# Performance work log

Measured on AMD Instinct MI355X. Metric: run time of the kernel, lower is better.

The kernel has to match this reference:

```python
import jax, jax.numpy as jnp
import numpy as np
import math

B, S, D_MODEL = 4, 2048, 1024
H, D_HEAD = 16, 64
INIT_RANGE = 0.02


def setup_inputs() -> dict:
    key = jax.random.key(0)
    ks = jax.random.split(key, 10)
    x = jax.random.normal(ks[0], (B, S, D_MODEL), dtype=jnp.float32)
    # torch Linear(in,out): y = x @ W.T + b. We store weights pre-transposed as [H, in, out].
    u = lambda k, shape: jax.random.uniform(k, shape, dtype=jnp.float32, minval=-INIT_RANGE, maxval=INIT_RANGE)
    wq = u(ks[1], (H, D_MODEL, D_HEAD))
    wk = u(ks[2], (H, D_MODEL, D_HEAD))
    wv = u(ks[3], (H, D_MODEL, D_HEAD))
    wo = u(ks[4], (H, D_HEAD, D_MODEL))
    # biases: torch default init is uniform(-1/sqrt(fan_in), 1/sqrt(fan_in)); values don't matter for correctness harness
    bq = u(ks[5], (H, D_HEAD))
    bk = u(ks[6], (H, D_HEAD))
    bv = u(ks[7], (H, D_HEAD))
    bo = u(ks[8], (H, D_MODEL))
    return {"normalized_resid_pre": x, "wq": wq, "bq": bq, "wk": wk, "bk": bk,
            "wv": wv, "bv": bv, "wo": wo, "bo": bo}


def reference(normalized_resid_pre, wq, bq, wk, bk, wv, bv, wo, bo):
    x = normalized_resid_pre  # [B, S, D]
    # Batched multi-head QKV projections (original does a python loop per head)
    q = jnp.einsum('bsd,hde->bhse', x, wq) + bq[None, :, None, :]  # [B,H,S,dh]
    k = jnp.einsum('bsd,hde->bhse', x, wk) + bk[None, :, None, :]
    v = jnp.einsum('bsd,hde->bhse', x, wv) + bv[None, :, None, :]
    scale = 1.0 / math.sqrt(D_HEAD)  # cfg.global_d_head, used unconditionally
    scores = jnp.einsum('bhse,bhte->bhst', q, k) * scale  # [B,H,S,S], non-causal
    attn = jax.nn.softmax(scores, axis=-1)
    heads = jnp.einsum('bhst,bhte->bhse', attn, v)  # [B,H,S,dh]
    # per-head output projections, summed over heads (= sum of per-head Linear outputs)
    out = jnp.einsum('bhse,hed->bsd', heads, wo) + jnp.sum(bo, axis=0)[None, None, :]
    return out
```

## Files before the change

### kernel.cpp

```cpp
#include <hip/hip_runtime.h>
#include <hip/hip_bf16.h>
#include <math.h>


typedef __attribute__((ext_vector_type(8))) short bf16x8;
typedef __attribute__((ext_vector_type(4))) float f32x4;

#define GLDS16(gsrc, lbase) \
    __builtin_amdgcn_global_load_lds((const __attribute__((address_space(1))) void*)(gsrc), \
                                     (__attribute__((address_space(3))) void*)(lbase), 16, 0, 0)

static __device__ __forceinline__ ushort f2bf(float f) {
    __bf16 h = (__bf16)f;
    return *reinterpret_cast<ushort*>(&h);
}
static __device__ __forceinline__ unsigned pk_bf16(float a, float b) {
    return (unsigned)f2bf(a) | ((unsigned)f2bf(b) << 16);
}
static __device__ __forceinline__ float clampf(float v) {
    return fminf(fmaxf(v, -1e30f), 1e30f);
}

__global__ void cvt_x(const float* __restrict__ x, ushort* __restrict__ xb) {
    int idx = blockIdx.x * 256 + threadIdx.x;
    float4 a = ((const float4*)x)[idx * 2];
    float4 b = ((const float4*)x)[idx * 2 + 1];
    uint4 o;
    o.x = pk_bf16(a.x, a.y);
    o.y = pk_bf16(a.z, a.w);
    o.z = pk_bf16(b.x, b.y);
    o.w = pk_bf16(b.z, b.w);
    ((uint4*)xb)[idx] = o;
}

__global__ void pack_wqkv(const float* __restrict__ wq, const float* __restrict__ wk,
                          const float* __restrict__ wv, const float* __restrict__ bq,
                          const float* __restrict__ bk, const float* __restrict__ bv,
                          ushort* __restrict__ WT, float* __restrict__ biasc) {
    __shared__ __align__(16) ushort Lt[64][72];
    int bid = blockIdx.x;
    int kt = bid & 15, h = (bid >> 4) & 15, proj = bid >> 8;
    const float* w  = (proj == 0) ? wq : (proj == 1) ? wk : wv;
    const float* bb = (proj == 0) ? bq : (proj == 1) ? bk : bv;
    const float scale = (proj == 0) ? 0.18033688011112042f : 1.0f;
    int t = threadIdx.x;
    int e = t & 63, kr = t >> 6;
    const float* src = w + (size_t)h * 65536 + (size_t)kt * 64 * 64 + e;
    #pragma unroll
    for (int i = 0; i < 16; ++i) {
        int kl = kr * 16 + i;
        Lt[e][kl] = f2bf(src[(size_t)kl * 64] * scale);
    }
    if (kt == 0 && t < 64) biasc[proj * 1024 + h * 64 + t] = bb[h * 64 + t] * scale;
    __syncthreads();
    int eo = t >> 2, kc = (t & 3) * 16;
    size_t dst = (size_t)(proj * 1024 + h * 64 + eo) * 1024 + kt * 64 + kc;
    *(bf16x8*)(WT + dst)     = *(const bf16x8*)(&Lt[eo][kc]);
    *(bf16x8*)(WT + dst + 8) = *(const bf16x8*)(&Lt[eo][kc + 8]);
}
__global__ void pack_wo(const float* __restrict__ wo, const float* __restrict__ bo,
                        ushort* __restrict__ WoT, float* __restrict__ biaso) {
    __shared__ __align__(16) ushort Lt[64][72];
    int bid = blockIdx.x;
    int het = bid & 15, dt = bid >> 4;
    int t = threadIdx.x;
    int dl = t & 63, hw = t >> 6;
    #pragma unroll
    for (int i = 0; i < 16; ++i) {
        int hel = hw * 16 + i;
        Lt[dl][hel] = f2bf(wo[(size_t)(het * 64 + hel) * 1024 + dt * 64 + dl]);
    }
    if (het == 0 && t < 64) {
        int d = dt * 64 + t;
        float s = 0.f;
        for (int hh = 0; hh < 16; ++hh) s += bo[hh * 1024 + d];
        biaso[d] = s;
    }
    __syncthreads();
    int do_ = t >> 2, hc = (t & 3) * 16;
    size_t dst = (size_t)(dt * 64 + do_) * 1024 + het * 64 + hc;
    *(bf16x8*)(WoT + dst)     = *(const bf16x8*)(&Lt[do_][hc]);
    *(bf16x8*)(WoT + dst + 8) = *(const bf16x8*)(&Lt[do_][hc + 8]);
}

__global__ void transpose_v(const ushort* __restrict__ C1x, ushort* __restrict__ Vt) {
    __shared__ ushort Lt[64][72];
    int st = blockIdx.x, b = blockIdx.y, h = blockIdx.z;
    int t = threadIdx.x;
    int r = t >> 3, c = (t & 7) * 8;
    #pragma unroll
    for (int i = 0; i < 2; ++i) {
        int sl = r + i * 32;
        bf16x8 v = *(const bf16x8*)(C1x + (size_t)(b * 2048 + st * 64 + sl) * 3072
                                    + 2048 + h * 64 + c);
        int pos = ((sl & 15) << 2) | (sl >> 4);
        #pragma unroll
        for (int j = 0; j < 8; ++j) Lt[c + j][pos] = (ushort)v[j];
    }
    __syncthreads();
    int e = t >> 2, ch = (t & 3) * 16;
    size_t dst = (size_t)b * (1024 * 2048) + (size_t)(h * 64 + e) * 2048 + st * 64 + ch;
    *(bf16x8*)(Vt + dst)     = *(const bf16x8*)(&Lt[e][ch]);
    *(bf16x8*)(Vt + dst + 8) = *(const bf16x8*)(&Lt[e][ch + 8]);
}

__global__ __launch_bounds__(256, 2) void gemm_bt(
    const ushort* __restrict__ A, const ushort* __restrict__ Bt,
    const float* __restrict__ bias, ushort* __restrict__ C,
    float* __restrict__ Cf, int M, int N, int K, int ldc)
{
    __shared__ __align__(16) ushort Al[128][64];
    __shared__ __align__(16) ushort Bl[128][64];
    const int t = threadIdx.x;
    const int lane = t & 63, wave = t >> 6;
    const int wr = wave >> 1, wc = wave & 1;
    const int quad = lane >> 4, l16 = lane & 15;
    const int row0 = blockIdx.x * 128, col0 = blockIdx.y * 128;
    const int sr = t >> 3;
    const int scx = ((t & 7) ^ (sr & 7)) * 8;
    const int xk = l16 & 7;

    f32x4 acc[4][4] = {};

    for (int kt = 0; kt < K; kt += 64) {
        char* abase = (char*)Al + wave * 1024;
        char* bbase = (char*)Bl + wave * 1024;
        const ushort* ag = A  + (size_t)(row0 + sr) * K + kt + scx;
        const ushort* bg = Bt + (size_t)(col0 + sr) * K + kt + scx;
        #pragma unroll
        for (int i = 0; i < 4; ++i) {
            GLDS16(ag + (size_t)i * 32 * K, abase + i * 4096);
            GLDS16(bg + (size_t)i * 32 * K, bbase + i * 4096);
        }
        __syncthreads();
        #pragma unroll
        for (int ks = 0; ks < 2; ++ks) {
            bf16x8 a[4], b[4];
            #pragma unroll
            for (int mi = 0; mi < 4; ++mi)
                a[mi] = *(const bf16x8*)(&Al[wr * 64 + mi * 16 + l16][((ks * 4 + quad) ^ xk) * 8]);
            #pragma unroll
            for (int ni = 0; ni < 4; ++ni)
                b[ni] = *(const bf16x8*)(&Bl[wc * 64 + ni * 16 + l16][((ks * 4 + quad) ^ xk) * 8]);
            #pragma unroll
            for (int mi = 0; mi < 4; ++mi)
                #pragma unroll
                for (int ni = 0; ni < 4; ++ni)
                    acc[mi][ni] = __builtin_amdgcn_mfma_f32_16x16x32_bf16(a[mi], b[ni], acc[mi][ni], 0, 0, 0);
        }
        __syncthreads();
    }
    #pragma unroll
    for (int mi = 0; mi < 4; ++mi) {
        int rowb = row0 + wr * 64 + mi * 16 + quad * 4;
        #pragma unroll
        for (int ni = 0; ni < 4; ++ni) {
            int col = col0 + wc * 64 + ni * 16 + l16;
            float bs = bias ? bias[col] : 0.f;
            #pragma unroll
            for (int r = 0; r < 4; ++r) {
                float v = clampf(acc[mi][ni][r] + bs);
                int row = rowb + r;
                if (Cf) Cf[(size_t)row * ldc + col] = v;
                else    C [(size_t)row * ldc + col] = f2bf(v);
            }
        }
    }
}

__global__ __launch_bounds__(256, 2) void attn(
    const ushort* __restrict__ QK, const ushort* __restrict__ Vt, ushort* __restrict__ O)
{
    __shared__ __align__(16) ushort Kl[64][64];
    __shared__ __align__(16) ushort Vl[64][64];
    __shared__ __align__(16) ushort Pl[4][32][72];
    const int qt = blockIdx.x, b = blockIdx.y, h = blockIdx.z;
    const int t = threadIdx.x, lane = t & 63, wave = t >> 6;
    const int quad = lane >> 4, l16 = lane & 15;
    const int rowq0 = b * 2048 + qt * 128 + wave * 32;
    const int sr = t >> 3;
    const int scx = ((t & 7) ^ (sr & 7)) * 8;
    const int xk = l16 & 7;

    bf16x8 qf[2][2];
    #pragma unroll
    for (int mi = 0; mi < 2; ++mi)
        #pragma unroll
        for (int ks = 0; ks < 2; ++ks)
            qf[mi][ks] = *(const bf16x8*)(QK + (size_t)(rowq0 + mi * 16 + l16) * 3072
                                          + h * 64 + ks * 32 + quad * 8);

    f32x4 of[2][4] = {};
    float lpart[2][4] = {};

    const ushort* kg0 = QK + (size_t)(b * 2048 + sr) * 3072 + 1024 + h * 64 + scx;
    const ushort* vg0 = Vt + (size_t)b * (1024 * 2048) + (size_t)(h * 64 + sr) * 2048 + scx;

    for (int kt = 0; kt < 2048; kt += 64) {
        {
            char* kbase = (char*)Kl + wave * 1024;
            char* vbase = (char*)Vl + wave * 1024;
            const ushort* kg = kg0 + (size_t)kt * 3072;
            const ushort* vg = vg0 + kt;
            GLDS16(kg, kbase);
            GLDS16(kg + (size_t)32 * 3072, kbase + 4096);
            GLDS16(vg, vbase);
            GLDS16(vg + 32 * 2048, vbase + 4096);
        }
        __syncthreads();

        f32x4 sf[2][4] = {};
        #pragma unroll
        for (int ks = 0; ks < 2; ++ks) {
            bf16x8 kb[4];
            #pragma unroll
            for (int nt = 0; nt < 4; ++nt)
                kb[nt] = *(const bf16x8*)(&Kl[nt * 16 + l16][((ks * 4 + quad) ^ xk) * 8]);
            #pragma unroll
            for (int mi = 0; mi < 2; ++mi)
                #pragma unroll
                for (int nt = 0; nt < 4; ++nt)
                    sf[mi][nt] = __builtin_amdgcn_mfma_f32_16x16x32_bf16(qf[mi][ks], kb[nt], sf[mi][nt], 0, 0, 0);
        }

        #pragma unroll
        for (int mi = 0; mi < 2; ++mi) {
            #pragma unroll
            for (int r = 0; r < 4; ++r) {
                float p0 = exp2f(sf[mi][0][r]);
                float p1 = exp2f(sf[mi][1][r]);
                float p2 = exp2f(sf[mi][2][r]);
                float p3 = exp2f(sf[mi][3][r]);
                lpart[mi][r] += (p0 + p1) + (p2 + p3);
                int prw = mi * 16 + quad * 4 + r;
                uint2 pk;
                pk.x = pk_bf16(p0, p1);
                pk.y = pk_bf16(p2, p3);
                *(uint2*)(&Pl[wave][prw][l16 * 4]) = pk;
            }
        }

        #pragma unroll
        for (int ks = 0; ks < 2; ++ks) {
            bf16x8 pa[2];
            #pragma unroll
            for (int mi = 0; mi < 2; ++mi)
                pa[mi] = *(const bf16x8*)(&Pl[wave][mi * 16 + l16][ks * 32 + quad * 8]);
            #pragma unroll
            for (int nt = 0; nt < 4; ++nt) {
                bf16x8 vb = *(const bf16x8*)(&Vl[nt * 16 + l16][((ks * 4 + quad) ^ xk) * 8]);
                #pragma unroll
                for (int mi = 0; mi < 2; ++mi)
                    of[mi][nt] = __builtin_amdgcn_mfma_f32_16x16x32_bf16(pa[mi], vb, of[mi][nt], 0, 0, 0);
            }
        }
        __syncthreads();
    }

    #pragma unroll
    for (int mi = 0; mi < 2; ++mi) {
        #pragma unroll
        for (int r = 0; r < 4; ++r) {
            float l = lpart[mi][r];
            #pragma unroll
            for (int d = 1; d < 16; d <<= 1) l += __shfl_xor(l, d, 64);
            float inv = 1.0f / fmaxf(l, 1e-30f);
            int row = rowq0 + mi * 16 + quad * 4 + r;
            #pragma unroll
            for (int nt = 0; nt < 4; ++nt)
                O[(size_t)row * 1024 + h * 64 + nt * 16 + l16] = f2bf(clampf(of[mi][nt][r] * inv));
        }
    }
}

extern "C" void kernel_launch(void* const* d_in, const int* in_sizes, int n_in,
                              void* d_out, int out_size, void* d_ws, size_t ws_size,
                              hipStream_t stream) {
    const float* x  = (const float*)d_in[0];
    const float* wq = (const float*)d_in[1];
    const float* bq = (const float*)d_in[2];
    const float* wk = (const float*)d_in[3];
    const float* bk = (const float*)d_in[4];
    const float* wv = (const float*)d_in[5];
    const float* bv = (const float*)d_in[6];
    const float* wo = (const float*)d_in[7];
    const float* bo = (const float*)d_in[8];

    char* ws = (char*)d_ws;
    const size_t MB = 1024 * 1024;
    ushort* xb    = (ushort*)(ws);
    ushort* WqkvT = (ushort*)(ws + 16 * MB);
    ushort* WoT   = (ushort*)(ws + 22 * MB);
    float*  biasc = (float*) (ws + 24 * MB);
    float*  biaso = (float*) (ws + 24 * MB + 64 * 1024);
    ushort* C1x   = (ushort*)(ws + 25 * MB);
    ushort* Vt    = (ushort*)(ws + 73 * MB);
    ushort* Obuf  = xb;

    cvt_x    <<<4096, 256, 0, stream>>>(x, xb);
    pack_wqkv<<<768, 256, 0, stream>>>(wq, wk, wv, bq, bk, bv, WqkvT, biasc);
    pack_wo  <<<256, 256, 0, stream>>>(wo, bo, WoT, biaso);

    gemm_bt<<<dim3(64, 24), 256, 0, stream>>>(xb, WqkvT, biasc, C1x, nullptr,
                                              8192, 3072, 1024, 3072);
    transpose_v<<<dim3(32, 4, 16), 256, 0, stream>>>(C1x, Vt);
    attn<<<dim3(16, 4, 16), 256, 0, stream>>>(C1x, Vt, Obuf);
    gemm_bt<<<dim3(64, 8), 256, 0, stream>>>(Obuf, WoT, biaso, nullptr, (float*)d_out,
                                             8192, 1024, 1024, 1024);
}
```

Measured before the change: 323.6 us.

## Enlarge attention blocks to 8 waves with 128-key tiles; fuse prep kernels

The attention kernel now runs 512 threads (8 waves) per block, covering 256 query rows, and stages 128 keys of K and V per iteration, processed in two 64-key halves. Each loaded K/V tile is shared by twice as many query rows, and there are half as many block-wide barriers per key. The three preprocessing kernels (x conversion, QKV weight pack, Wo pack) are merged into one launch to cut launch overhead. The trade-offs are more LDS per block, a new swizzle for the wider V tile, and fewer blocks in the grid, which may reduce occupancy.

Result: slower. 457.2 us (+41.3%).

```diff
diff --git a/kernel.cpp b/kernel.cpp
--- a/kernel.cpp
+++ b/kernel.cpp
@@ -21,66 +21,70 @@
     return fminf(fmaxf(v, -1e30f), 1e30f);
 }
 
-__global__ void cvt_x(const float* __restrict__ x, ushort* __restrict__ xb) {
-    int idx = blockIdx.x * 256 + threadIdx.x;
-    float4 a = ((const float4*)x)[idx * 2];
-    float4 b = ((const float4*)x)[idx * 2 + 1];
-    uint4 o;
-    o.x = pk_bf16(a.x, a.y);
-    o.y = pk_bf16(a.z, a.w);
-    o.z = pk_bf16(b.x, b.y);
-    o.w = pk_bf16(b.z, b.w);
-    ((uint4*)xb)[idx] = o;
-}
-
-__global__ void pack_wqkv(const float* __restrict__ wq, const float* __restrict__ wk,
-                          const float* __restrict__ wv, const float* __restrict__ bq,
-                          const float* __restrict__ bk, const float* __restrict__ bv,
-                          ushort* __restrict__ WT, float* __restrict__ biasc) {
+__global__ void prep(const float* __restrict__ x, ushort* __restrict__ xb,
+                     const float* __restrict__ wq, const float* __restrict__ wk,
+                     const float* __restrict__ wv, const float* __restrict__ bq,
+                     const float* __restrict__ bk, const float* __restrict__ bv,
+                     ushort* __restrict__ WT, float* __restrict__ biasc,
+                     const float* __restrict__ wo, const float* __restrict__ bo,
+                     ushort* __restrict__ WoT, float* __restrict__ biaso) {
     __shared__ __align__(16) ushort Lt[64][72];
     int bid = blockIdx.x;
-    int kt = bid & 15, h = (bid >> 4) & 15, proj = bid >> 8;
-    const float* w  = (proj == 0) ? wq : (proj == 1) ? wk : wv;
-    const float* bb = (proj == 0) ? bq : (proj == 1) ? bk : bv;
-    const float scale = (proj == 0) ? 0.18033688011112042f : 1.0f;
     int t = threadIdx.x;
-    int e = t & 63, kr = t >> 6;
-    const float* src = w + (size_t)h * 65536 + (size_t)kt * 64 * 64 + e;
-    #pragma unroll
-    for (int i = 0; i < 16; ++i) {
-        int kl = kr * 16 + i;
-        Lt[e][kl] = f2bf(src[(size_t)kl * 64] * scale);
-    }
-    if (kt == 0 && t < 64) biasc[proj * 1024 + h * 64 + t] = bb[h * 64 + t] * scale;
-    __syncthreads();
-    int eo = t >> 2, kc = (t & 3) * 16;
-    size_t dst = (size_t)(proj * 1024 + h * 64 + eo) * 1024 + kt * 64 + kc;
-    *(bf16x8*)(WT + dst)     = *(const bf16x8*)(&Lt[eo][kc]);
-    *(bf16x8*)(WT + dst + 8) = *(const bf16x8*)(&Lt[eo][kc + 8]);
-}
-__global__ void pack_wo(const float* __restrict__ wo, const float* __restrict__ bo,
-                        ushort* __restrict__ WoT, float* __restrict__ biaso) {
-    __shared__ __align__(16) ushort Lt[64][72];
-    int bid = blockIdx.x;
-    int het = bid & 15, dt = bid >> 4;
-    int t = threadIdx.x;
-    int dl = t & 63, hw = t >> 6;
-    #pragma unroll
-    for (int i = 0; i < 16; ++i) {
-        int hel = hw * 16 + i;
-        Lt[dl][hel] = f2bf(wo[(size_t)(het * 64 + hel) * 1024 + dt * 64 + dl]);
-    }
-    if (het == 0 && t < 64) {
-        int d = dt * 64 + t;
-        float s = 0.f;
-        for (int hh = 0; hh < 16; ++hh) s += bo[hh * 1024 + d];
-        biaso[d] = s;
-    }
-    __syncthreads();
-    int do_ = t >> 2, hc = (t & 3) * 16;
-    size_t dst = (size_t)(dt * 64 + do_) * 1024 + het * 64 + hc;
-    *(bf16x8*)(WoT + dst)     = *(const bf16x8*)(&Lt[do_][hc]);
-    *(bf16x8*)(WoT + dst + 8) = *(const bf16x8*)(&Lt[do_][hc + 8]);
+    if (bid < 4096) {
+        int idx = bid * 256 + t;
+        float4 a = ((const float4*)x)[idx * 2];
+        float4 b = ((const float4*)x)[idx * 2 + 1];
+        uint4 o;
+        o.x = pk_bf16(a.x, a.y);
+        o.y = pk_bf16(a.z, a.w);
+        o.z = pk_bf16(b.x, b.y);
+        o.w = pk_bf16(b.z, b.w);
+        ((uint4*)xb)[idx] = o;
+        return;
+    }
+    bid -= 4096;
+    if (bid < 768) {
+        int kt = bid & 15, h = (bid >> 4) & 15, proj = bid >> 8;
+        const float* w  = (proj == 0) ? wq : (proj == 1) ? wk : wv;
+        const float* bb = (proj == 0) ? bq : (proj == 1) ? bk : bv;
+        const float scale = (proj == 0) ? 0.18033688011112042f : 1.0f;
+        int e = t & 63, kr = t >> 6;
+        const float* src = w + (size_t)h * 65536 + (size_t)kt * 64 * 64 + e;
+        #pragma unroll
+        for (int i = 0; i < 16; ++i) {
+            int kl = kr * 16 + i;
+            Lt[e][kl] = f2bf(src[(size_t)kl * 64] * scale);
+        }
+        if (kt == 0 && t < 64) biasc[proj * 1024 + h * 64 + t] = bb[h * 64 + t] * scale;
+        __syncthreads();
+        int eo = t >> 2, kc = (t & 3) * 16;
+        size_t dst = (size_t)(proj * 1024 + h * 64 + eo) * 1024 + kt * 64 + kc;
+        *(bf16x8*)(WT + dst)     = *(const bf16x8*)(&Lt[eo][kc]);
+        *(bf16x8*)(WT + dst + 8) = *(const bf16x8*)(&Lt[eo][kc + 8]);
+        return;
+    }
+    bid -= 768;
+    {
+        int het = bid & 15, dt = bid >> 4;
+        int dl = t & 63, hw = t >> 6;
+        #pragma unroll
+        for (int i = 0; i < 16; ++i) {
+            int hel = hw * 16 + i;
+            Lt[dl][hel] = f2bf(wo[(size_t)(het * 64 + hel) * 1024 + dt * 64 + dl]);
+        }
+        if (het == 0 && t < 64) {
+            int d = dt * 64 + t;
+            float s = 0.f;
+            for (int hh = 0; hh < 16; ++hh) s += bo[hh * 1024 + d];
+            biaso[d] = s;
+        }
+        __syncthreads();
+        int do_ = t >> 2, hc = (t & 3) * 16;
+        size_t dst = (size_t)(dt * 64 + do_) * 1024 + het * 64 + hc;
+        *(bf16x8*)(WoT + dst)     = *(const bf16x8*)(&Lt[do_][hc]);
+        *(bf16x8*)(WoT + dst + 8) = *(const bf16x8*)(&Lt[do_][hc + 8]);
+    }
 }
 
 __global__ void transpose_v(const ushort* __restrict__ C1x, ushort* __restrict__ Vt) {
@@ -168,18 +172,16 @@
     }
 }
 
-__global__ __launch_bounds__(256, 2) void attn(
+__global__ __launch_bounds__(512, 4) void attn(
     const ushort* __restrict__ QK, const ushort* __restrict__ Vt, ushort* __restrict__ O)
 {
-    __shared__ __align__(16) ushort Kl[64][64];
-    __shared__ __align__(16) ushort Vl[64][64];
-    __shared__ __align__(16) ushort Pl[4][32][72];
+    __shared__ __align__(16) ushort Kl[128][64];
+    __shared__ __align__(16) ushort Vl[64][128];
+    __shared__ __align__(16) ushort Pl[8][32][72];
     const int qt = blockIdx.x, b = blockIdx.y, h = blockIdx.z;
     const int t = threadIdx.x, lane = t & 63, wave = t >> 6;
     const int quad = lane >> 4, l16 = lane & 15;
-    const int rowq0 = b * 2048 + qt * 128 + wave * 32;
-    const int sr = t >> 3;
-    const int scx = ((t & 7) ^ (sr & 7)) * 8;
+    const int rowq0 = b * 2048 + qt * 256 + wave * 32;
     const int xk = l16 & 7;
 
     bf16x8 qf[2][2];
@@ -193,65 +195,68 @@
     f32x4 of[2][4] = {};
     float lpart[2][4] = {};
 
-    const ushort* kg0 = QK + (size_t)(b * 2048 + sr) * 3072 + 1024 + h * 64 + scx;
-    const ushort* vg0 = Vt + (size_t)b * (1024 * 2048) + (size_t)(h * 64 + sr) * 2048 + scx;
-
-    for (int kt = 0; kt < 2048; kt += 64) {
-        {
-            char* kbase = (char*)Kl + wave * 1024;
-            char* vbase = (char*)Vl + wave * 1024;
-            const ushort* kg = kg0 + (size_t)kt * 3072;
-            const ushort* vg = vg0 + kt;
-            GLDS16(kg, kbase);
-            GLDS16(kg + (size_t)32 * 3072, kbase + 4096);
-            GLDS16(vg, vbase);
-            GLDS16(vg + 32 * 2048, vbase + 4096);
-        }
-        __syncthreads();
-
-        f32x4 sf[2][4] = {};
-        #pragma unroll
-        for (int ks = 0; ks < 2; ++ks) {
-            bf16x8 kb[4];
-            #pragma unroll
-            for (int nt = 0; nt < 4; ++nt)
-                kb[nt] = *(const bf16x8*)(&Kl[nt * 16 + l16][((ks * 4 + quad) ^ xk) * 8]);
-            #pragma unroll
-            for (int mi = 0; mi < 2; ++mi)
+    const int krow = wave * 8 + (lane >> 3);
+    const int ksc  = ((lane & 7) ^ (lane >> 3)) * 8;
+    const ushort* kg0 = QK + (size_t)(b * 2048 + krow) * 3072 + 1024 + h * 64 + ksc;
+    const int vrow = wave * 4 + (lane >> 4);
+    const int vsc  = ((lane & 15) ^ (vrow & 15)) * 8;
+    const ushort* vg0 = Vt + (size_t)b * (1024 * 2048) + (size_t)(h * 64 + vrow) * 2048 + vsc;
+    char* kbase = (char*)Kl + wave * 1024;
+    char* vbase = (char*)Vl + wave * 1024;
+
+    for (int kt = 0; kt < 2048; kt += 128) {
+        GLDS16(kg0 + (size_t)kt * 3072,        kbase);
+        GLDS16(kg0 + (size_t)(kt + 64) * 3072, kbase + 8192);
+        GLDS16(vg0 + kt,                        vbase);
+        GLDS16(vg0 + kt + 32 * 2048,            vbase + 8192);
+        __syncthreads();
+
+        #pragma unroll
+        for (int hf = 0; hf < 2; ++hf) {
+            f32x4 sf[2][4] = {};
+            #pragma unroll
+            for (int ks = 0; ks < 2; ++ks) {
+                bf16x8 kb[4];
                 #pragma unroll
                 for (int nt = 0; nt < 4; ++nt)
-                    sf[mi][nt] = __builtin_amdgcn_mfma_f32_16x16x32_bf16(qf[mi][ks], kb[nt], sf[mi][nt], 0, 0, 0);
-        }
-
-        #pragma unroll
-        for (int mi = 0; mi < 2; ++mi) {
-            #pragma unroll
-            for (int r = 0; r < 4; ++r) {
-                float p0 = exp2f(sf[mi][0][r]);
-                float p1 = exp2f(sf[mi][1][r]);
-                float p2 = exp2f(sf[mi][2][r]);
-                float p3 = exp2f(sf[mi][3][r]);
-                lpart[mi][r] += (p0 + p1) + (p2 + p3);
-                int prw = mi * 16 + quad * 4 + r;
-                uint2 pk;
-                pk.x = pk_bf16(p0, p1);
-                pk.y = pk_bf16(p2, p3);
-                *(uint2*)(&Pl[wave][prw][l16 * 4]) = pk;
+                    kb[nt] = *(const bf16x8*)(&Kl[hf * 64 + nt * 16 + l16][((ks * 4 + quad) ^ xk) * 8]);
+                #pragma unroll
+                for (int mi = 0; mi < 2; ++mi)
+                    #pragma unroll
+                    for (int nt = 0; nt < 4; ++nt)
+                        sf[mi][nt] = __builtin_amdgcn_mfma_f32_16x16x32_bf16(qf[mi][ks], kb[nt], sf[mi][nt], 0, 0, 0);
             }
-        }
-
-        #pragma unroll
-        for (int ks = 0; ks < 2; ++ks) {
-            bf16x8 pa[2];
-            #pragma unroll
-            for (int mi = 0; mi < 2; ++mi)
-                pa[mi] = *(const bf16x8*)(&Pl[wave][mi * 16 + l16][ks * 32 + quad * 8]);
-            #pragma unroll
-            for (int nt = 0; nt < 4; ++nt) {
-                bf16x8 vb = *(const bf16x8*)(&Vl[nt * 16 + l16][((ks * 4 + quad) ^ xk) * 8]);
+
+            #pragma unroll
+            for (int mi = 0; mi < 2; ++mi) {
+                #pragma unroll
+                for (int r = 0; r < 4; ++r) {
+                    float p0 = exp2f(sf[mi][0][r]);
+                    float p1 = exp2f(sf[mi][1][r]);
+                    float p2 = exp2f(sf[mi][2][r]);
+                    float p3 = exp2f(sf[mi][3][r]);
+                    lpart[mi][r] += (p0 + p1) + (p2 + p3);
+                    int prw = mi * 16 + quad * 4 + r;
+                    uint2 pk;
+                    pk.x = pk_bf16(p0, p1);
+                    pk.y = pk_bf16(p2, p3);
+                    *(uint2*)(&Pl[wave][prw][l16 * 4]) = pk;
+                }
+            }
+
+            #pragma unroll
+            for (int ks = 0; ks < 2; ++ks) {
+                bf16x8 pa[2];
                 #pragma unroll
                 for (int mi = 0; mi < 2; ++mi)
-                    of[mi][nt] = __builtin_amdgcn_mfma_f32_16x16x32_bf16(pa[mi], vb, of[mi][nt], 0, 0, 0);
+                    pa[mi] = *(const bf16x8*)(&Pl[wave][mi * 16 + l16][ks * 32 + quad * 8]);
+                #pragma unroll
+                for (int nt = 0; nt < 4; ++nt) {
+                    bf16x8 vb = *(const bf16x8*)(&Vl[nt * 16 + l16][((hf * 8 + ks * 4 + quad) ^ l16) * 8]);
+                    #pragma unroll
+                    for (int mi = 0; mi < 2; ++mi)
+                        of[mi][nt] = __builtin_amdgcn_mfma_f32_16x16x32_bf16(pa[mi], vb, of[mi][nt], 0, 0, 0);
+                }
             }
         }
         __syncthreads();
@@ -297,14 +302,12 @@
     ushort* Vt    = (ushort*)(ws + 73 * MB);
     ushort* Obuf  = xb;
 
-    cvt_x    <<<4096, 256, 0, stream>>>(x, xb);
-    pack_wqkv<<<768, 256, 0, stream>>>(wq, wk, wv, bq, bk, bv, WqkvT, biasc);
-    pack_wo  <<<256, 256, 0, stream>>>(wo, bo, WoT, biaso);
-
+    prep<<<5120, 256, 0, stream>>>(x, xb, wq, wk, wv, bq, bk, bv, WqkvT, biasc,
+                                   wo, bo, WoT, biaso);
     gemm_bt<<<dim3(64, 24), 256, 0, stream>>>(xb, WqkvT, biasc, C1x, nullptr,
                                               8192, 3072, 1024, 3072);
     transpose_v<<<dim3(32, 4, 16), 256, 0, stream>>>(C1x, Vt);
-    attn<<<dim3(16, 4, 16), 256, 0, stream>>>(C1x, Vt, Obuf);
+    attn<<<dim3(8, 4, 16), 512, 0, stream>>>(C1x, Vt, Obuf);
     gemm_bt<<<dim3(64, 8), 256, 0, stream>>>(Obuf, WoT, biaso, nullptr, (float*)d_out,
                                              8192, 1024, 1024, 1024);
 }
```
